# Kernel tuning notes

Measured on AMD Instinct MI355X. Metric: run time of the kernel, lower is better.

## Reference

```python
import jax, jax.numpy as jnp
import numpy as np

B, S, H, NH = 32, 577, 1024, 16
DH = H // NH


def setup_inputs() -> dict:
    key = jax.random.key(0)
    ks = jax.random.split(key, 10)
    s = 0.02
    return {
        "hidden_states": jax.random.normal(ks[0], (B, S, H), dtype=jnp.float32),
        "attention_mask": jnp.ones((B, S), dtype=jnp.float32),
        "Wq": jax.random.normal(ks[1], (H, H), dtype=jnp.float32) * s,
        "bq": jnp.zeros((H,), dtype=jnp.float32),
        "Wk": jax.random.normal(ks[2], (H, H), dtype=jnp.float32) * s,
        "bk": jnp.zeros((H,), dtype=jnp.float32),
        "Wv": jax.random.normal(ks[3], (H, H), dtype=jnp.float32) * s,
        "bv": jnp.zeros((H,), dtype=jnp.float32),
        "Wo": jax.random.normal(ks[4], (H, H), dtype=jnp.float32) * s,
        "bo": jnp.zeros((H,), dtype=jnp.float32),
    }


def reference(hidden_states, attention_mask, Wq, bq, Wk, bk, Wv, bv, Wo, bo):
    # torch nn.Linear: y = x @ W.T + b
    def heads(x):  # [B,S,H] -> [B,NH,S,DH]
        return x.reshape(B, S, NH, DH).transpose(0, 2, 1, 3)

    q = heads(hidden_states @ Wq.T + bq)
    k = heads(hidden_states @ Wk.T + bk)
    v = heads(hidden_states @ Wv.T + bv)

    scores = jnp.einsum("bhqd,bhkd->bhqk", q, k) / jnp.sqrt(jnp.float32(DH))
    # multiplicative mask, broadcast over heads and query positions
    scores = scores * attention_mask[:, None, None, :]
    probs = jax.nn.softmax(scores, axis=-1)
    ctx = jnp.einsum("bhqk,bhkd->bhqd", probs, v)
    ctx = ctx.transpose(0, 2, 1, 3).reshape(B, S, H)
    return ctx @ Wo.T + bo
```

## Files before the change

### kernel.cpp

```cpp
#include <hip/hip_runtime.h>
#include <hip/hip_bf16.h>


typedef __bf16 bf16_t;
typedef __bf16 bf16x8 __attribute__((ext_vector_type(8)));
typedef __bf16 bf16x4 __attribute__((ext_vector_type(4)));
typedef float f32x4 __attribute__((ext_vector_type(4)));

#define B_   32
#define S_   577
#define SP   608
#define H_   1024
#define NH_  16
#define DH_  64
#define M_   (B_ * S_)

typedef __attribute__((address_space(3))) unsigned int lds_u32;
typedef const __attribute__((address_space(1))) unsigned int glb_u32;
#define STAGE16(gp, lp) __builtin_amdgcn_global_load_lds((glb_u32*)(gp), (lds_u32*)(lp), 16, 0, 0)

__device__ __forceinline__ bf16x8 load8(const bf16_t* p) {
    return *reinterpret_cast<const bf16x8*>(p);
}
__device__ __forceinline__ bf16x8 load8f(const float* p) {
    f32x4 a = *reinterpret_cast<const f32x4*>(p);
    f32x4 b = *reinterpret_cast<const f32x4*>(p + 4);
    bf16x8 r;
    r[0] = (bf16_t)a[0]; r[1] = (bf16_t)a[1]; r[2] = (bf16_t)a[2]; r[3] = (bf16_t)a[3];
    r[4] = (bf16_t)b[0]; r[5] = (bf16_t)b[1]; r[6] = (bf16_t)b[2]; r[7] = (bf16_t)b[3];
    return r;
}

__global__ __launch_bounds__(256) void cvt_f32_bf16(const float* __restrict__ src,
                                                    bf16_t* __restrict__ dst, int n8)
{
    int i = blockIdx.x * blockDim.x + threadIdx.x;
    const int stride = gridDim.x * blockDim.x;
    for (; i < n8; i += stride)
        *reinterpret_cast<bf16x8*>(dst + (size_t)i * 8) = load8f(src + (size_t)i * 8);
}

__global__ __launch_bounds__(256) void cvt_w4(
    const float* __restrict__ s0, const float* __restrict__ s1,
    const float* __restrict__ s2, const float* __restrict__ s3,
    bf16_t* __restrict__ dst)
{
    const int i = blockIdx.x * blockDim.x + threadIdx.x;
    const int which = i >> 17;
    const int off = i & ((1 << 17) - 1);
    const float* s = (which == 0) ? s0 : (which == 1) ? s1 : (which == 2) ? s2 : s3;
    *reinterpret_cast<bf16x8*>(dst + (size_t)i * 8) = load8f(s + (size_t)off * 8);
}

#define GEMM_MAINLOOP(SWAP)                                                      \
    for (int k0 = 0; k0 < H_; k0 += 32) {                                        \
        STAGE16(pA0 + k0, lA0);                                                  \
        STAGE16(pA1 + k0, lA1);                                                  \
        STAGE16(pB0 + k0, lB0);                                                  \
        STAGE16(pB1 + k0, lB1);                                                  \
        __syncthreads();                                                         \
        bf16x8 af[4], bfv[4];                                                    \
        _Pragma("unroll")                                                        \
        for (int tt = 0; tt < 4; ++tt) {                                         \
            af[tt]  = load8(sA + (wm * 64 + tt * 16 + l16) * 32 + quad * 8);     \
            bfv[tt] = load8(sB + (wn * 64 + tt * 16 + l16) * 32 + quad * 8);     \
        }                                                                        \
        _Pragma("unroll")                                                        \
        for (int i = 0; i < 4; ++i)                                              \
            _Pragma("unroll")                                                    \
            for (int j = 0; j < 4; ++j)                                          \
                acc[i][j] = (SWAP)                                               \
                    ? __builtin_amdgcn_mfma_f32_16x16x32_bf16(bfv[j], af[i], acc[i][j], 0, 0, 0) \
                    : __builtin_amdgcn_mfma_f32_16x16x32_bf16(af[i], bfv[j], acc[i][j], 0, 0, 0); \
        __syncthreads();                                                         \
    }

__global__ __launch_bounds__(256) void qkv_gemm(
    const bf16_t* __restrict__ Xb,
    const bf16_t* __restrict__ Wqb, const bf16_t* __restrict__ Wkb, const bf16_t* __restrict__ Wvb,
    const float* __restrict__ bq, const float* __restrict__ bk, const float* __restrict__ bv,
    bf16_t* __restrict__ Qb, bf16_t* __restrict__ Kb, bf16_t* __restrict__ VTb)
{
    __shared__ bf16_t smem[8192];
    bf16_t* sA = smem;
    bf16_t* sB = smem + 4096;
    const int tid  = threadIdx.x;
    const int w    = tid >> 6, lane = tid & 63;
    const int quad = lane >> 4, l16 = lane & 15;
    const int wm = w & 1, wn = w >> 1;

    const int t    = (blockIdx.x & 7) * 435 + (blockIdx.x >> 3);
    const int slab = t / 192;
    const int rem  = t - slab * 192;
    int mt, nt;
    if (slab < 18) { nt = rem >> 3; mt = slab * 8 + (rem & 7); }
    else           { nt = rem;      mt = 144; }
    const int m0 = mt * 128, n0 = nt * 128;

    const int which = n0 >> 10;
    const int nrel0 = n0 & 1023;
    const bf16_t* Wb   = (which == 0) ? Wqb : (which == 1) ? Wkb : Wvb;
    const float*  bias = (which == 0) ? bq  : (which == 1) ? bk  : bv;
    const float   oscale = (which == 0) ? 0.125f : 1.0f;

    const int f0 = tid, f1 = 256 + tid;
    const int rA0 = f0 >> 2, cA0 = (f0 & 3) * 8;
    const int rA1 = f1 >> 2, cA1 = (f1 & 3) * 8;
    int ga0 = m0 + rA0; if (ga0 > M_ - 1) ga0 = M_ - 1;
    int ga1 = m0 + rA1; if (ga1 > M_ - 1) ga1 = M_ - 1;
    const bf16_t* pA0 = Xb + (size_t)ga0 * H_ + cA0;
    const bf16_t* pA1 = Xb + (size_t)ga1 * H_ + cA1;
    const bf16_t* pB0 = Wb + (size_t)(nrel0 + rA0) * H_ + cA0;
    const bf16_t* pB1 = Wb + (size_t)(nrel0 + rA1) * H_ + cA1;
    bf16_t* lA0 = sA + w * 512;
    bf16_t* lA1 = sA + 2048 + w * 512;
    bf16_t* lB0 = sB + w * 512;
    bf16_t* lB1 = sB + 2048 + w * 512;

    f32x4 acc[4][4] = {};
    if (which != 2) {
        GEMM_MAINLOOP(1)
        bf16_t* QKout = (which == 0) ? Qb : Kb;
#pragma unroll
        for (int j = 0; j < 4; ++j) {
            const int u  = wn * 4 + j;
            const int h  = (nrel0 >> 6) + (u >> 2);
            const int d0 = (u & 3) * 16 + quad * 4;
            const f32x4 b4 = *reinterpret_cast<const f32x4*>(&bias[nrel0 + u * 16 + quad * 4]);
#pragma unroll
            for (int i = 0; i < 4; ++i) {
                const int m = m0 + wm * 64 + i * 16 + l16;
                if (m >= M_) continue;
                const int b = m / S_, s = m - b * S_;
                const int bh = b * NH_ + h;
                bf16x4 pk;
#pragma unroll
                for (int r = 0; r < 4; ++r) pk[r] = (bf16_t)((acc[i][j][r] + b4[r]) * oscale);
                *reinterpret_cast<bf16x4*>(QKout + ((size_t)bh * S_ + s) * DH_ + d0) = pk;
            }
        }
    } else {
        GEMM_MAINLOOP(0)
#pragma unroll
        for (int j = 0; j < 4; ++j) {
            const int nrel = nrel0 + wn * 64 + j * 16 + l16;
            const float bv_ = bias[nrel];
            const int h = nrel >> 6, d = nrel & 63;
#pragma unroll
            for (int i = 0; i < 4; ++i) {
                const int m = m0 + wm * 64 + i * 16 + quad * 4;
                const int b = m / S_, s = m - b * S_;
                if (m + 3 < M_ && s <= S_ - 4) {
                    bf16x4 pk;
#pragma unroll
                    for (int r = 0; r < 4; ++r) pk[r] = (bf16_t)(acc[i][j][r] + bv_);
                    *reinterpret_cast<bf16x4*>(VTb + ((size_t)(b * NH_ + h) * DH_ + d) * SP + s) = pk;
                } else {
#pragma unroll
                    for (int r = 0; r < 4; ++r) {
                        const int mm = m + r;
                        if (mm >= M_) continue;
                        const int bb = mm / S_, ss = mm - bb * S_;
                        VTb[((size_t)(bb * NH_ + h) * DH_ + d) * SP + ss] = (bf16_t)(acc[i][j][r] + bv_);
                    }
                }
            }
        }
    }
}

__global__ __launch_bounds__(256, 3) void flash_attn(
    const bf16_t* __restrict__ Qb, const bf16_t* __restrict__ Kb,
    const bf16_t* __restrict__ VTb, const float* __restrict__ maskp,
    bf16_t* __restrict__ Ctx)
{
    __shared__ __align__(16) float smask[SP];
    const int tid  = threadIdx.x;
    const int w    = tid >> 6, lane = tid & 63;
    const int quad = lane >> 4, l16 = lane & 15;

    const int bid  = blockIdx.x;
    const int work = (bid & 7) * 320 + (bid >> 3);
    const int bh   = work / 5;
    const int qx   = work - bh * 5;
    const int b    = bh >> 4, h = bh & 15;

    for (int i = tid; i < SP; i += 256)
        smask[i] = (i < S_) ? maskp[b * S_ + i] : 0.f;
    __syncthreads();

    int idx = qx * 4 + w; if (idx > 18) idx = 18;
    const int q0 = idx * 32;

    const bf16_t* Qh = Qb  + (size_t)bh * S_ * DH_;
    const bf16_t* Kh = Kb  + (size_t)bh * S_ * DH_;
    const bf16_t* Vh = VTb + (size_t)bh * DH_ * SP;

    int rqA = q0 + l16;      if (rqA > S_ - 1) rqA = S_ - 1;
    int rqB = q0 + 16 + l16; if (rqB > S_ - 1) rqB = S_ - 1;
    const bf16x8 aqA0 = load8(Qh + rqA * DH_ + quad * 8);
    const bf16x8 aqA1 = load8(Qh + rqA * DH_ + 32 + quad * 8);
    const bf16x8 aqB0 = load8(Qh + rqB * DH_ + quad * 8);
    const bf16x8 aqB1 = load8(Qh + rqB * DH_ + 32 + quad * 8);

    const int g0 = ((l16 >> 2) << 3) + (l16 & 3);
    const int g1 = g0 + 4;

    f32x4 oA[4] = {}, oB[4] = {};
    float lpA = 0.f, lpB = 0.f;

    bf16x8 ka[4], kb_[4];
    {
        int r0 = g0; if (r0 > S_ - 1) r0 = S_ - 1;
        int r1 = g1; if (r1 > S_ - 1) r1 = S_ - 1;
        ka[0] = load8(Kh + r0 * DH_ + quad * 8);
        ka[1] = load8(Kh + r0 * DH_ + 32 + quad * 8);
        ka[2] = load8(Kh + r1 * DH_ + quad * 8);
        ka[3] = load8(Kh + r1 * DH_ + 32 + quad * 8);
    }

    auto body = [&](bf16x8 (&KC)[4], bf16x8 (&KN)[4], const int j0, const bool pf) {
        bf16x8 v0 = load8(Vh + (l16)      * SP + j0 + quad * 8);
        bf16x8 v1 = load8(Vh + (16 + l16) * SP + j0 + quad * 8);
        bf16x8 v2 = load8(Vh + (32 + l16) * SP + j0 + quad * 8);
        bf16x8 v3 = load8(Vh + (48 + l16) * SP + j0 + quad * 8);
        if (pf) {
            int r0 = j0 + 32 + g0; if (r0 > S_ - 1) r0 = S_ - 1;
            int r1 = j0 + 32 + g1; if (r1 > S_ - 1) r1 = S_ - 1;
            KN[0] = load8(Kh + r0 * DH_ + quad * 8);
            KN[1] = load8(Kh + r0 * DH_ + 32 + quad * 8);
            KN[2] = load8(Kh + r1 * DH_ + quad * 8);
            KN[3] = load8(Kh + r1 * DH_ + 32 + quad * 8);
        }
        f32x4 sA0 = {}, sA1 = {}, sB0 = {}, sB1 = {};
        sA0 = __builtin_amdgcn_mfma_f32_16x16x32_bf16(KC[0], aqA0, sA0, 0, 0, 0);
        sA0 = __builtin_amdgcn_mfma_f32_16x16x32_bf16(KC[1], aqA1, sA0, 0, 0, 0);
        sA1 = __builtin_amdgcn_mfma_f32_16x16x32_bf16(KC[2], aqA0, sA1, 0, 0, 0);
        sA1 = __builtin_amdgcn_mfma_f32_16x16x32_bf16(KC[3], aqA1, sA1, 0, 0, 0);
        sB0 = __builtin_amdgcn_mfma_f32_16x16x32_bf16(KC[0], aqB0, sB0, 0, 0, 0);
        sB0 = __builtin_amdgcn_mfma_f32_16x16x32_bf16(KC[1], aqB1, sB0, 0, 0, 0);
        sB1 = __builtin_amdgcn_mfma_f32_16x16x32_bf16(KC[2], aqB0, sB1, 0, 0, 0);
        sB1 = __builtin_amdgcn_mfma_f32_16x16x32_bf16(KC[3], aqB1, sB1, 0, 0, 0);

        const f32x4 mk0 = *reinterpret_cast<const f32x4*>(&smask[j0 + quad * 8]);
        const f32x4 mk1 = *reinterpret_cast<const f32x4*>(&smask[j0 + quad * 8 + 4]);
        bf16x8 apA, apB;
#pragma unroll
        for (int r = 0; r < 4; ++r) {
            const int c0 = j0 + quad * 8 + r;
            const int c1 = c0 + 4;
            const float eA0 = (c0 < S_) ? __expf(sA0[r] * mk0[r]) : 0.f;
            const float eA1 = (c1 < S_) ? __expf(sA1[r] * mk1[r]) : 0.f;
            const float eB0 = (c0 < S_) ? __expf(sB0[r] * mk0[r]) : 0.f;
            const float eB1 = (c1 < S_) ? __expf(sB1[r] * mk1[r]) : 0.f;
            lpA += eA0 + eA1;
            lpB += eB0 + eB1;
            apA[r] = (bf16_t)eA0; apA[r + 4] = (bf16_t)eA1;
            apB[r] = (bf16_t)eB0; apB[r + 4] = (bf16_t)eB1;
        }
        oA[0] = __builtin_amdgcn_mfma_f32_16x16x32_bf16(apA, v0, oA[0], 0, 0, 0);
        oB[0] = __builtin_amdgcn_mfma_f32_16x16x32_bf16(apB, v0, oB[0], 0, 0, 0);
        oA[1] = __builtin_amdgcn_mfma_f32_16x16x32_bf16(apA, v1, oA[1], 0, 0, 0);
        oB[1] = __builtin_amdgcn_mfma_f32_16x16x32_bf16(apB, v1, oB[1], 0, 0, 0);
        oA[2] = __builtin_amdgcn_mfma_f32_16x16x32_bf16(apA, v2, oA[2], 0, 0, 0);
        oB[2] = __builtin_amdgcn_mfma_f32_16x16x32_bf16(apB, v2, oB[2], 0, 0, 0);
        oA[3] = __builtin_amdgcn_mfma_f32_16x16x32_bf16(apA, v3, oA[3], 0, 0, 0);
        oB[3] = __builtin_amdgcn_mfma_f32_16x16x32_bf16(apB, v3, oB[3], 0, 0, 0);
    };

    for (int j0 = 0; j0 < S_; j0 += 64) {
        body(ka, kb_, j0, j0 + 32 < S_);
        if (j0 + 32 < S_) body(kb_, ka, j0 + 32, j0 + 64 < S_);
    }

    float lsA = lpA, lsB = lpB;
    lsA += __shfl_xor(lsA, 16); lsA += __shfl_xor(lsA, 32);
    lsB += __shfl_xor(lsB, 16); lsB += __shfl_xor(lsB, 32);
    float livA[4], livB[4];
#pragma unroll
    for (int r = 0; r < 4; ++r) {
        livA[r] = 1.0f / __shfl(lsA, quad * 4 + r);
        livB[r] = 1.0f / __shfl(lsB, quad * 4 + r);
    }

#pragma unroll
    for (int t = 0; t < 4; ++t) {
#pragma unroll
        for (int r = 0; r < 4; ++r) {
            const int sA = q0 + quad * 4 + r;
            const int sB = sA + 16;
            if (sA < S_)
                Ctx[((size_t)(b * S_ + sA) * NH_ + h) * DH_ + t * 16 + l16] =
                    (bf16_t)(oA[t][r] * livA[r]);
            if (sB < S_)
                Ctx[((size_t)(b * S_ + sB) * NH_ + h) * DH_ + t * 16 + l16] =
                    (bf16_t)(oB[t][r] * livB[r]);
        }
    }
}

__global__ __launch_bounds__(256) void out_gemm(
    const bf16_t* __restrict__ Ctx, const bf16_t* __restrict__ Wob,
    const float* __restrict__ bo, float* __restrict__ Out)
{
    __shared__ bf16_t smem[8192];
    bf16_t* sA = smem;
    bf16_t* sB = smem + 4096;
    const int tid  = threadIdx.x;
    const int w    = tid >> 6, lane = tid & 63;
    const int quad = lane >> 4, l16 = lane & 15;
    const int wm = w & 1, wn = w >> 1;

    const int t    = (blockIdx.x & 7) * 145 + (blockIdx.x >> 3);
    const int slab = t / 64;
    const int rem  = t - slab * 64;
    int mt, nt;
    if (slab < 18) { nt = rem >> 3; mt = slab * 8 + (rem & 7); }
    else           { nt = rem;      mt = 144; }
    const int m0 = mt * 128, n0 = nt * 128;

    const int f0 = tid, f1 = 256 + tid;
    const int rA0 = f0 >> 2, cA0 = (f0 & 3) * 8;
    const int rA1 = f1 >> 2, cA1 = (f1 & 3) * 8;
    int ga0 = m0 + rA0; if (ga0 > M_ - 1) ga0 = M_ - 1;
    int ga1 = m0 + rA1; if (ga1 > M_ - 1) ga1 = M_ - 1;
    const bf16_t* pA0 = Ctx + (size_t)ga0 * H_ + cA0;
    const bf16_t* pA1 = Ctx + (size_t)ga1 * H_ + cA1;
    const bf16_t* pB0 = Wob + (size_t)(n0 + rA0) * H_ + cA0;
    const bf16_t* pB1 = Wob + (size_t)(n0 + rA1) * H_ + cA1;
    bf16_t* lA0 = sA + w * 512;
    bf16_t* lA1 = sA + 2048 + w * 512;
    bf16_t* lB0 = sB + w * 512;
    bf16_t* lB1 = sB + 2048 + w * 512;

    f32x4 acc[4][4] = {};
    GEMM_MAINLOOP(1)

#pragma unroll
    for (int j = 0; j < 4; ++j) {
        const int nb = n0 + wn * 64 + j * 16 + quad * 4;
        const f32x4 b4 = *reinterpret_cast<const f32x4*>(&bo[nb]);
#pragma unroll
        for (int i = 0; i < 4; ++i) {
            const int m = m0 + wm * 64 + i * 16 + l16;
            if (m >= M_) continue;
            f32x4 v = acc[i][j] + b4;
            *reinterpret_cast<f32x4*>(Out + (size_t)m * H_ + nb) = v;
        }
    }
}

extern "C" void kernel_launch(void* const* d_in, const int* in_sizes, int n_in,
                              void* d_out, int out_size, void* d_ws, size_t ws_size,
                              hipStream_t stream) {
    const float* hidden = (const float*)d_in[0];
    const float* mask   = (const float*)d_in[1];
    const float* Wq = (const float*)d_in[2];
    const float* bq = (const float*)d_in[3];
    const float* Wk = (const float*)d_in[4];
    const float* bk = (const float*)d_in[5];
    const float* Wv = (const float*)d_in[6];
    const float* bv = (const float*)d_in[7];
    const float* Wo = (const float*)d_in[8];
    const float* bo = (const float*)d_in[9];
    float* out = (float*)d_out;

    const size_t QK_EL = (size_t)B_ * NH_ * S_ * DH_;
    const size_t VT_EL = (size_t)B_ * NH_ * SP * DH_;
    const size_t X_EL  = (size_t)M_ * H_;
    const size_t W_EL  = (size_t)H_ * H_;
    const size_t NEED  = (2 * QK_EL + VT_EL + X_EL + 4 * W_EL) * sizeof(bf16_t);
    if (ws_size < NEED) {
        hipMemsetAsync(d_out, 0, (size_t)out_size * sizeof(float), stream);
        return;
    }

    bf16_t* ws    = (bf16_t*)d_ws;
    bf16_t* Qb    = ws;
    bf16_t* Kb    = Qb + QK_EL;
    bf16_t* VTb   = Kb + QK_EL;
    bf16_t* XbCtx = VTb + VT_EL;
    bf16_t* Wqb   = XbCtx + X_EL;
    bf16_t* Wkb   = Wqb + W_EL;
    bf16_t* Wvb   = Wkb + W_EL;
    bf16_t* Wob   = Wvb + W_EL;

    cvt_f32_bf16<<<2048, 256, 0, stream>>>(hidden, XbCtx, (int)(X_EL / 8));
    cvt_w4<<<2048, 256, 0, stream>>>(Wq, Wk, Wv, Wo, Wqb);

    qkv_gemm<<<dim3(3480), dim3(256), 0, stream>>>(XbCtx, Wqb, Wkb, Wvb, bq, bk, bv, Qb, Kb, VTb);

    flash_attn<<<dim3(2560), dim3(256), 0, stream>>>(Qb, Kb, VTb, mask, XbCtx);

    out_gemm<<<dim3(1160), dim3(256), 0, stream>>>(XbCtx, Wob, bo, out);
}
```

Before: 504.9 us.

## Double-buffer LDS staging in GEMMs and raise wave priority around attention MFMAs

The GEMM main loop now uses two LDS buffers, so the global-to-LDS load for the next K-slice is issued before the MFMAs on the current slice run, and one of the two barriers per step is removed. Shared memory per block doubles to 32 KB, which may lower occupancy. The attention kernel also wraps its MFMA groups in s_setprio(1)/s_setprio(0) so waves issuing matrix work are favoured by the scheduler over waves doing softmax and loads.

```diff
diff --git a/kernel.cpp b/kernel.cpp
--- a/kernel.cpp
+++ b/kernel.cpp
@@ -52,18 +52,21 @@
     *reinterpret_cast<bf16x8*>(dst + (size_t)i * 8) = load8f(s + (size_t)off * 8);
 }
 
-#define GEMM_MAINLOOP(SWAP)                                                      \
-    for (int k0 = 0; k0 < H_; k0 += 32) {                                        \
-        STAGE16(pA0 + k0, lA0);                                                  \
-        STAGE16(pA1 + k0, lA1);                                                  \
-        STAGE16(pB0 + k0, lB0);                                                  \
-        STAGE16(pB1 + k0, lB1);                                                  \
-        __syncthreads();                                                         \
+#define GEMM_STAGE(base, kofs)                                                   \
+    do {                                                                         \
+        STAGE16(pA0 + (kofs), (base) + w * 512);                                 \
+        STAGE16(pA1 + (kofs), (base) + 2048 + w * 512);                          \
+        STAGE16(pB0 + (kofs), (base) + 4096 + w * 512);                          \
+        STAGE16(pB1 + (kofs), (base) + 6144 + w * 512);                          \
+    } while (0)
+
+#define GEMM_COMPUTE(base, SWAP)                                                 \
+    do {                                                                         \
         bf16x8 af[4], bfv[4];                                                    \
         _Pragma("unroll")                                                        \
         for (int tt = 0; tt < 4; ++tt) {                                         \
-            af[tt]  = load8(sA + (wm * 64 + tt * 16 + l16) * 32 + quad * 8);     \
-            bfv[tt] = load8(sB + (wn * 64 + tt * 16 + l16) * 32 + quad * 8);     \
+            af[tt]  = load8((base) + (wm * 64 + tt * 16 + l16) * 32 + quad * 8); \
+            bfv[tt] = load8((base) + 4096 + (wn * 64 + tt * 16 + l16) * 32 + quad * 8); \
         }                                                                        \
         _Pragma("unroll")                                                        \
         for (int i = 0; i < 4; ++i)                                              \
@@ -72,6 +75,17 @@
                 acc[i][j] = (SWAP)                                               \
                     ? __builtin_amdgcn_mfma_f32_16x16x32_bf16(bfv[j], af[i], acc[i][j], 0, 0, 0) \
                     : __builtin_amdgcn_mfma_f32_16x16x32_bf16(af[i], bfv[j], acc[i][j], 0, 0, 0); \
+    } while (0)
+
+#define GEMM_MAINLOOP(SWAP)                                                      \
+    GEMM_STAGE(smem, 0);                                                         \
+    __syncthreads();                                                             \
+    for (int kk = 0; kk < H_; kk += 64) {                                        \
+        GEMM_STAGE(smem + 8192, kk + 32);                                        \
+        GEMM_COMPUTE(smem, SWAP);                                                \
+        __syncthreads();                                                         \
+        if (kk + 64 < H_) GEMM_STAGE(smem, kk + 64);                             \
+        GEMM_COMPUTE(smem + 8192, SWAP);                                         \
         __syncthreads();                                                         \
     }
 
@@ -81,9 +95,7 @@
     const float* __restrict__ bq, const float* __restrict__ bk, const float* __restrict__ bv,
     bf16_t* __restrict__ Qb, bf16_t* __restrict__ Kb, bf16_t* __restrict__ VTb)
 {
-    __shared__ bf16_t smem[8192];
-    bf16_t* sA = smem;
-    bf16_t* sB = smem + 4096;
+    __shared__ bf16_t smem[16384];
     const int tid  = threadIdx.x;
     const int w    = tid >> 6, lane = tid & 63;
     const int quad = lane >> 4, l16 = lane & 15;
@@ -112,10 +124,6 @@
     const bf16_t* pA1 = Xb + (size_t)ga1 * H_ + cA1;
     const bf16_t* pB0 = Wb + (size_t)(nrel0 + rA0) * H_ + cA0;
     const bf16_t* pB1 = Wb + (size_t)(nrel0 + rA1) * H_ + cA1;
-    bf16_t* lA0 = sA + w * 512;
-    bf16_t* lA1 = sA + 2048 + w * 512;
-    bf16_t* lB0 = sB + w * 512;
-    bf16_t* lB1 = sB + 2048 + w * 512;
 
     f32x4 acc[4][4] = {};
     if (which != 2) {
@@ -233,6 +241,7 @@
             KN[3] = load8(Kh + r1 * DH_ + 32 + quad * 8);
         }
         f32x4 sA0 = {}, sA1 = {}, sB0 = {}, sB1 = {};
+        __builtin_amdgcn_s_setprio(1);
         sA0 = __builtin_amdgcn_mfma_f32_16x16x32_bf16(KC[0], aqA0, sA0, 0, 0, 0);
         sA0 = __builtin_amdgcn_mfma_f32_16x16x32_bf16(KC[1], aqA1, sA0, 0, 0, 0);
         sA1 = __builtin_amdgcn_mfma_f32_16x16x32_bf16(KC[2], aqA0, sA1, 0, 0, 0);
@@ -241,6 +250,7 @@
         sB0 = __builtin_amdgcn_mfma_f32_16x16x32_bf16(KC[1], aqB1, sB0, 0, 0, 0);
         sB1 = __builtin_amdgcn_mfma_f32_16x16x32_bf16(KC[2], aqB0, sB1, 0, 0, 0);
         sB1 = __builtin_amdgcn_mfma_f32_16x16x32_bf16(KC[3], aqB1, sB1, 0, 0, 0);
+        __builtin_amdgcn_s_setprio(0);
 
         const f32x4 mk0 = *reinterpret_cast<const f32x4*>(&smask[j0 + quad * 8]);
         const f32x4 mk1 = *reinterpret_cast<const f32x4*>(&smask[j0 + quad * 8 + 4]);
@@ -258,6 +268,7 @@
             apA[r] = (bf16_t)eA0; apA[r + 4] = (bf16_t)eA1;
             apB[r] = (bf16_t)eB0; apB[r + 4] = (bf16_t)eB1;
         }
+        __builtin_amdgcn_s_setprio(1);
         oA[0] = __builtin_amdgcn_mfma_f32_16x16x32_bf16(apA, v0, oA[0], 0, 0, 0);
         oB[0] = __builtin_amdgcn_mfma_f32_16x16x32_bf16(apB, v0, oB[0], 0, 0, 0);
         oA[1] = __builtin_amdgcn_mfma_f32_16x16x32_bf16(apA, v1, oA[1], 0, 0, 0);
@@ -266,6 +277,7 @@
         oB[2] = __builtin_amdgcn_mfma_f32_16x16x32_bf16(apB, v2, oB[2], 0, 0, 0);
         oA[3] = __builtin_amdgcn_mfma_f32_16x16x32_bf16(apA, v3, oA[3], 0, 0, 0);
         oB[3] = __builtin_amdgcn_mfma_f32_16x16x32_bf16(apB, v3, oB[3], 0, 0, 0);
+        __builtin_amdgcn_s_setprio(0);
     };
 
     for (int j0 = 0; j0 < S_; j0 += 64) {
@@ -303,9 +315,7 @@
     const bf16_t* __restrict__ Ctx, const bf16_t* __restrict__ Wob,
     const float* __restrict__ bo, float* __restrict__ Out)
 {
-    __shared__ bf16_t smem[8192];
-    bf16_t* sA = smem;
-    bf16_t* sB = smem + 4096;
+    __shared__ bf16_t smem[16384];
     const int tid  = threadIdx.x;
     const int w    = tid >> 6, lane = tid & 63;
     const int quad = lane >> 4, l16 = lane & 15;
@@ -328,10 +338,6 @@
     const bf16_t* pA1 = Ctx + (size_t)ga1 * H_ + cA1;
     const bf16_t* pB0 = Wob + (size_t)(n0 + rA0) * H_ + cA0;
     const bf16_t* pB1 = Wob + (size_t)(n0 + rA1) * H_ + cA1;
-    bf16_t* lA0 = sA + w * 512;
-    bf16_t* lA1 = sA + 2048 + w * 512;
-    bf16_t* lB0 = sB + w * 512;
-    bf16_t* lB1 = sB + 2048 + w * 512;
 
     f32x4 acc[4][4] = {};
     GEMM_MAINLOOP(1)
```

New measurement: 507.7 us. Within noise of the previous version (+0.6%).

## Rewrite QKV GEMM with 256x256 tiles and multi-stage async LDS pipeline

Applied to the files above, without the earlier changes.

Replaces the QKV projection GEMM's 128x128 single-buffered main loop with a 256x256 tile using 512 threads and a four-slot LDS ring (two K-halves by two parities). Global-to-LDS loads for future steps are issued while MFMAs run, and waits use explicit vmcnt counts instead of full syncthreads. The grid is remapped across XCDs to match the new tile count. s_setprio is also raised around the MFMA bursts in the GEMM and the flash attention kernel. The larger tile cuts load traffic per FLOP and hides load latency, at the cost of 128KB of LDS and higher register pressure, which may lower occupancy.

```diff
diff --git a/kernel.cpp b/kernel.cpp
--- a/kernel.cpp
+++ b/kernel.cpp
@@ -18,6 +18,7 @@
 typedef __attribute__((address_space(3))) unsigned int lds_u32;
 typedef const __attribute__((address_space(1))) unsigned int glb_u32;
 #define STAGE16(gp, lp) __builtin_amdgcn_global_load_lds((glb_u32*)(gp), (lds_u32*)(lp), 16, 0, 0)
+#define MFMA_BF16 __builtin_amdgcn_mfma_f32_16x16x32_bf16
 
 __device__ __forceinline__ bf16x8 load8(const bf16_t* p) {
     return *reinterpret_cast<const bf16x8*>(p);
@@ -52,50 +53,91 @@
     *reinterpret_cast<bf16x8*>(dst + (size_t)i * 8) = load8f(s + (size_t)off * 8);
 }
 
-#define GEMM_MAINLOOP(SWAP)                                                      \
-    for (int k0 = 0; k0 < H_; k0 += 32) {                                        \
-        STAGE16(pA0 + k0, lA0);                                                  \
-        STAGE16(pA1 + k0, lA1);                                                  \
-        STAGE16(pB0 + k0, lB0);                                                  \
-        STAGE16(pB1 + k0, lB1);                                                  \
-        __syncthreads();                                                         \
-        bf16x8 af[4], bfv[4];                                                    \
+#define AR(par, kk) (((par) * 2 + (kk)) * 8192)
+#define BR(par, kk) (32768 + ((par) * 2 + (kk)) * 8192)
+
+#define STG_A(par, kk, T)                                                        \
+    do {                                                                         \
+        STAGE16(pA0 + (T) * 64 + (kk) * 32, smem + AR(par, kk) + w * 512);       \
+        STAGE16(pA1 + (T) * 64 + (kk) * 32, smem + AR(par, kk) + 4096 + w * 512);\
+    } while (0)
+#define STG_B(par, kk, T)                                                        \
+    do {                                                                         \
+        STAGE16(pB0 + (T) * 64 + (kk) * 32, smem + BR(par, kk) + w * 512);       \
+        STAGE16(pB1 + (T) * 64 + (kk) * 32, smem + BR(par, kk) + 4096 + w * 512);\
+    } while (0)
+
+#define PHASE_A(par, kk, STG, SWAP)                                              \
+    do {                                                                         \
+        asm volatile("s_waitcnt vmcnt(8)" ::: "memory");                         \
+        __builtin_amdgcn_s_barrier();                                            \
+        STG;                                                                     \
         _Pragma("unroll")                                                        \
-        for (int tt = 0; tt < 4; ++tt) {                                         \
-            af[tt]  = load8(sA + (wm * 64 + tt * 16 + l16) * 32 + quad * 8);     \
-            bfv[tt] = load8(sB + (wn * 64 + tt * 16 + l16) * 32 + quad * 8);     \
+        for (int i = 0; i < 8; ++i)                                              \
+            af[i] = load8(smem + AR(par, kk) + (wr * 128 + i * 16 + l16) * 32 + quad * 8); \
+        bfv[0] = load8(smem + BR(par, kk) + (wc * 64 + l16) * 32 + quad * 8);    \
+        bfv[1] = load8(smem + BR(par, kk) + (wc * 64 + 16 + l16) * 32 + quad * 8); \
+        __builtin_amdgcn_s_setprio(1);                                           \
+        _Pragma("unroll")                                                        \
+        for (int i = 0; i < 8; ++i) {                                            \
+            acc[i][0] = (SWAP) ? MFMA_BF16(bfv[0], af[i], acc[i][0], 0, 0, 0)    \
+                               : MFMA_BF16(af[i], bfv[0], acc[i][0], 0, 0, 0);   \
+            acc[i][1] = (SWAP) ? MFMA_BF16(bfv[1], af[i], acc[i][1], 0, 0, 0)    \
+                               : MFMA_BF16(af[i], bfv[1], acc[i][1], 0, 0, 0);   \
         }                                                                        \
+        __builtin_amdgcn_s_setprio(0);                                           \
+    } while (0)
+
+#define PHASE_B(par, kk, STG, SWAP)                                              \
+    do {                                                                         \
+        STG;                                                                     \
+        bfv[2] = load8(smem + BR(par, kk) + (wc * 64 + 32 + l16) * 32 + quad * 8); \
+        bfv[3] = load8(smem + BR(par, kk) + (wc * 64 + 48 + l16) * 32 + quad * 8); \
+        __builtin_amdgcn_s_setprio(1);                                           \
         _Pragma("unroll")                                                        \
-        for (int i = 0; i < 4; ++i)                                              \
-            _Pragma("unroll")                                                    \
-            for (int j = 0; j < 4; ++j)                                          \
-                acc[i][j] = (SWAP)                                               \
-                    ? __builtin_amdgcn_mfma_f32_16x16x32_bf16(bfv[j], af[i], acc[i][j], 0, 0, 0) \
-                    : __builtin_amdgcn_mfma_f32_16x16x32_bf16(af[i], bfv[j], acc[i][j], 0, 0, 0); \
-        __syncthreads();                                                         \
-    }
-
-__global__ __launch_bounds__(256) void qkv_gemm(
+        for (int i = 0; i < 8; ++i) {                                            \
+            acc[i][2] = (SWAP) ? MFMA_BF16(bfv[2], af[i], acc[i][2], 0, 0, 0)    \
+                               : MFMA_BF16(af[i], bfv[2], acc[i][2], 0, 0, 0);   \
+            acc[i][3] = (SWAP) ? MFMA_BF16(bfv[3], af[i], acc[i][3], 0, 0, 0)    \
+                               : MFMA_BF16(af[i], bfv[3], acc[i][3], 0, 0, 0);   \
+        }                                                                        \
+        __builtin_amdgcn_s_setprio(0);                                           \
+    } while (0)
+
+#define QKV_MAIN(SWAP)                                                           \
+    STG_A(0, 0, 0); STG_B(0, 0, 0); STG_A(0, 1, 0); STG_B(0, 1, 0);              \
+    STG_A(1, 0, 1); STG_B(1, 0, 1);                                              \
+    for (int it = 0; it < 8; ++it) {                                             \
+        const int t1 = 2 * it + 1;                                               \
+        const int t2 = (2 * it + 2 < 16) ? 2 * it + 2 : 15;                      \
+        const int t3 = (2 * it + 3 < 16) ? 2 * it + 3 : 15;                      \
+        PHASE_A(0, 0, STG_A(1, 1, t1), SWAP); PHASE_B(0, 0, STG_B(1, 1, t1), SWAP); \
+        PHASE_A(0, 1, STG_A(0, 0, t2), SWAP); PHASE_B(0, 1, STG_B(0, 0, t2), SWAP); \
+        PHASE_A(1, 0, STG_A(0, 1, t2), SWAP); PHASE_B(1, 0, STG_B(0, 1, t2), SWAP); \
+        PHASE_A(1, 1, STG_A(1, 0, t3), SWAP); PHASE_B(1, 1, STG_B(1, 0, t3), SWAP); \
+    }                                                                            \
+    asm volatile("s_waitcnt vmcnt(0)" ::: "memory");
+
+__global__ __launch_bounds__(512, 2) void qkv_gemm(
     const bf16_t* __restrict__ Xb,
     const bf16_t* __restrict__ Wqb, const bf16_t* __restrict__ Wkb, const bf16_t* __restrict__ Wvb,
     const float* __restrict__ bq, const float* __restrict__ bk, const float* __restrict__ bv,
     bf16_t* __restrict__ Qb, bf16_t* __restrict__ Kb, bf16_t* __restrict__ VTb)
 {
-    __shared__ bf16_t smem[8192];
-    bf16_t* sA = smem;
-    bf16_t* sB = smem + 4096;
+    __shared__ bf16_t smem[65536];
     const int tid  = threadIdx.x;
     const int w    = tid >> 6, lane = tid & 63;
     const int quad = lane >> 4, l16 = lane & 15;
-    const int wm = w & 1, wn = w >> 1;
-
-    const int t    = (blockIdx.x & 7) * 435 + (blockIdx.x >> 3);
-    const int slab = t / 192;
-    const int rem  = t - slab * 192;
+    const int wr = w >> 2, wc = w & 3;
+
+    const int orig = blockIdx.x;
+    const int xcd = orig & 7, lin = orig >> 3;
+    const int work = (xcd < 4 ? xcd * 110 : 440 + (xcd - 4) * 109) + lin;
     int mt, nt;
-    if (slab < 18) { nt = rem >> 3; mt = slab * 8 + (rem & 7); }
-    else           { nt = rem;      mt = 144; }
-    const int m0 = mt * 128, n0 = nt * 128;
+    if (work < 864) { const int slab = work / 48, rem = work - slab * 48;
+                      nt = rem >> 2; mt = slab * 4 + (rem & 3); }
+    else            { nt = work - 864; mt = 72; }
+    const int m0 = mt * 256, n0 = nt * 256;
 
     const int which = n0 >> 10;
     const int nrel0 = n0 & 1023;
@@ -103,33 +145,28 @@
     const float*  bias = (which == 0) ? bq  : (which == 1) ? bk  : bv;
     const float   oscale = (which == 0) ? 0.125f : 1.0f;
 
-    const int f0 = tid, f1 = 256 + tid;
-    const int rA0 = f0 >> 2, cA0 = (f0 & 3) * 8;
-    const int rA1 = f1 >> 2, cA1 = (f1 & 3) * 8;
-    int ga0 = m0 + rA0; if (ga0 > M_ - 1) ga0 = M_ - 1;
-    int ga1 = m0 + rA1; if (ga1 > M_ - 1) ga1 = M_ - 1;
-    const bf16_t* pA0 = Xb + (size_t)ga0 * H_ + cA0;
-    const bf16_t* pA1 = Xb + (size_t)ga1 * H_ + cA1;
-    const bf16_t* pB0 = Wb + (size_t)(nrel0 + rA0) * H_ + cA0;
-    const bf16_t* pB1 = Wb + (size_t)(nrel0 + rA1) * H_ + cA1;
-    bf16_t* lA0 = sA + w * 512;
-    bf16_t* lA1 = sA + 2048 + w * 512;
-    bf16_t* lB0 = sB + w * 512;
-    bf16_t* lB1 = sB + 2048 + w * 512;
-
-    f32x4 acc[4][4] = {};
+    const int srow = tid >> 2, scol = (tid & 3) * 8;
+    int ga0 = m0 + srow;       if (ga0 > M_ - 1) ga0 = M_ - 1;
+    int ga1 = m0 + 128 + srow; if (ga1 > M_ - 1) ga1 = M_ - 1;
+    const bf16_t* pA0 = Xb + (size_t)ga0 * H_ + scol;
+    const bf16_t* pA1 = Xb + (size_t)ga1 * H_ + scol;
+    const bf16_t* pB0 = Wb + (size_t)(nrel0 + srow) * H_ + scol;
+    const bf16_t* pB1 = Wb + (size_t)(nrel0 + 128 + srow) * H_ + scol;
+
+    bf16x8 af[8], bfv[4];
+    f32x4 acc[8][4] = {};
+
     if (which != 2) {
-        GEMM_MAINLOOP(1)
+        QKV_MAIN(1)
         bf16_t* QKout = (which == 0) ? Qb : Kb;
 #pragma unroll
         for (int j = 0; j < 4; ++j) {
-            const int u  = wn * 4 + j;
-            const int h  = (nrel0 >> 6) + (u >> 2);
-            const int d0 = (u & 3) * 16 + quad * 4;
-            const f32x4 b4 = *reinterpret_cast<const f32x4*>(&bias[nrel0 + u * 16 + quad * 4]);
-#pragma unroll
-            for (int i = 0; i < 4; ++i) {
-                const int m = m0 + wm * 64 + i * 16 + l16;
+            const int nrelj = nrel0 + wc * 64 + j * 16 + quad * 4;
+            const int h = nrelj >> 6, d0 = nrelj & 63;
+            const f32x4 b4 = *reinterpret_cast<const f32x4*>(&bias[nrelj]);
+#pragma unroll
+            for (int i = 0; i < 8; ++i) {
+                const int m = m0 + wr * 128 + i * 16 + l16;
                 if (m >= M_) continue;
                 const int b = m / S_, s = m - b * S_;
                 const int bh = b * NH_ + h;
@@ -140,15 +177,15 @@
             }
         }
     } else {
-        GEMM_MAINLOOP(0)
+        QKV_MAIN(0)
 #pragma unroll
         for (int j = 0; j < 4; ++j) {
-            const int nrel = nrel0 + wn * 64 + j * 16 + l16;
-            const float bv_ = bias[nrel];
-            const int h = nrel >> 6, d = nrel & 63;
-#pragma unroll
-            for (int i = 0; i < 4; ++i) {
-                const int m = m0 + wm * 64 + i * 16 + quad * 4;
+            const int nrelj = nrel0 + wc * 64 + j * 16 + l16;
+            const int h = nrelj >> 6, d = nrelj & 63;
+            const float bv_ = bias[nrelj];
+#pragma unroll
+            for (int i = 0; i < 8; ++i) {
+                const int m = m0 + wr * 128 + i * 16 + quad * 4;
                 const int b = m / S_, s = m - b * S_;
                 if (m + 3 < M_ && s <= S_ - 4) {
                     bf16x4 pk;
@@ -233,14 +270,16 @@
             KN[3] = load8(Kh + r1 * DH_ + 32 + quad * 8);
         }
         f32x4 sA0 = {}, sA1 = {}, sB0 = {}, sB1 = {};
-        sA0 = __builtin_amdgcn_mfma_f32_16x16x32_bf16(KC[0], aqA0, sA0, 0, 0, 0);
-        sA0 = __builtin_amdgcn_mfma_f32_16x16x32_bf16(KC[1], aqA1, sA0, 0, 0, 0);
-        sA1 = __builtin_amdgcn_mfma_f32_16x16x32_bf16(KC[2], aqA0, sA1, 0, 0, 0);
-        sA1 = __builtin_amdgcn_mfma_f32_16x16x32_bf16(KC[3], aqA1, sA1, 0, 0, 0);
-        sB0 = __builtin_amdgcn_mfma_f32_16x16x32_bf16(KC[0], aqB0, sB0, 0, 0, 0);
-        sB0 = __builtin_amdgcn_mfma_f32_16x16x32_bf16(KC[1], aqB1, sB0, 0, 0, 0);
-        sB1 = __builtin_amdgcn_mfma_f32_16x16x32_bf16(KC[2], aqB0, sB1, 0, 0, 0);
-        sB1 = __builtin_amdgcn_mfma_f32_16x16x32_bf16(KC[3], aqB1, sB1, 0, 0, 0);
+        __builtin_amdgcn_s_setprio(1);
+        sA0 = MFMA_BF16(KC[0], aqA0, sA0, 0, 0, 0);
+        sA0 = MFMA_BF16(KC[1], aqA1, sA0, 0, 0, 0);
+        sA1 = MFMA_BF16(KC[2], aqA0, sA1, 0, 0, 0);
+        sA1 = MFMA_BF16(KC[3], aqA1, sA1, 0, 0, 0);
+        sB0 = MFMA_BF16(KC[0], aqB0, sB0, 0, 0, 0);
+        sB0 = MFMA_BF16(KC[1], aqB1, sB0, 0, 0, 0);
+        sB1 = MFMA_BF16(KC[2], aqB0, sB1, 0, 0, 0);
+        sB1 = MFMA_BF16(KC[3], aqB1, sB1, 0, 0, 0);
+        __builtin_amdgcn_s_setprio(0);
 
         const f32x4 mk0 = *reinterpret_cast<const f32x4*>(&smask[j0 + quad * 8]);
         const f32x4 mk1 = *reinterpret_cast<const f32x4*>(&smask[j0 + quad * 8 + 4]);
@@ -258,14 +297,16 @@
             apA[r] = (bf16_t)eA0; apA[r + 4] = (bf16_t)eA1;
             apB[r] = (bf16_t)eB0; apB[r + 4] = (bf16_t)eB1;
         }
-        oA[0] = __builtin_amdgcn_mfma_f32_16x16x32_bf16(apA, v0, oA[0], 0, 0, 0);
-        oB[0] = __builtin_amdgcn_mfma_f32_16x16x32_bf16(apB, v0, oB[0], 0, 0, 0);
-        oA[1] = __builtin_amdgcn_mfma_f32_16x16x32_bf16(apA, v1, oA[1], 0, 0, 0);
-        oB[1] = __builtin_amdgcn_mfma_f32_16x16x32_bf16(apB, v1, oB[1], 0, 0, 0);
-        oA[2] = __builtin_amdgcn_mfma_f32_16x16x32_bf16(apA, v2, oA[2], 0, 0, 0);
-        oB[2] = __builtin_amdgcn_mfma_f32_16x16x32_bf16(apB, v2, oB[2], 0, 0, 0);
-        oA[3] = __builtin_amdgcn_mfma_f32_16x16x32_bf16(apA, v3, oA[3], 0, 0, 0);
-        oB[3] = __builtin_amdgcn_mfma_f32_16x16x32_bf16(apB, v3, oB[3], 0, 0, 0);
+        __builtin_amdgcn_s_setprio(1);
+        oA[0] = MFMA_BF16(apA, v0, oA[0], 0, 0, 0);
+        oB[0] = MFMA_BF16(apB, v0, oB[0], 0, 0, 0);
+        oA[1] = MFMA_BF16(apA, v1, oA[1], 0, 0, 0);
+        oB[1] = MFMA_BF16(apB, v1, oB[1], 0, 0, 0);
+        oA[2] = MFMA_BF16(apA, v2, oA[2], 0, 0, 0);
+        oB[2] = MFMA_BF16(apB, v2, oB[2], 0, 0, 0);
+        oA[3] = MFMA_BF16(apA, v3, oA[3], 0, 0, 0);
+        oB[3] = MFMA_BF16(apB, v3, oB[3], 0, 0, 0);
+        __builtin_amdgcn_s_setprio(0);
     };
 
     for (int j0 = 0; j0 < S_; j0 += 64) {
@@ -334,7 +375,25 @@
     bf16_t* lB1 = sB + 2048 + w * 512;
 
     f32x4 acc[4][4] = {};
-    GEMM_MAINLOOP(1)
+    for (int k0 = 0; k0 < H_; k0 += 32) {
+        STAGE16(pA0 + k0, lA0);
+        STAGE16(pA1 + k0, lA1);
+        STAGE16(pB0 + k0, lB0);
+        STAGE16(pB1 + k0, lB1);
+        __syncthreads();
+        bf16x8 af[4], bfv[4];
+#pragma unroll
+        for (int tt = 0; tt < 4; ++tt) {
+            af[tt]  = load8(sA + (wm * 64 + tt * 16 + l16) * 32 + quad * 8);
+            bfv[tt] = load8(sB + (wn * 64 + tt * 16 + l16) * 32 + quad * 8);
+        }
+#pragma unroll
+        for (int i = 0; i < 4; ++i)
+#pragma unroll
+            for (int j = 0; j < 4; ++j)
+                acc[i][j] = MFMA_BF16(bfv[j], af[i], acc[i][j], 0, 0, 0);
+        __syncthreads();
+    }
 
 #pragma unroll
     for (int j = 0; j < 4; ++j) {
@@ -388,7 +447,7 @@
     cvt_f32_bf16<<<2048, 256, 0, stream>>>(hidden, XbCtx, (int)(X_EL / 8));
     cvt_w4<<<2048, 256, 0, stream>>>(Wq, Wk, Wv, Wo, Wqb);
 
-    qkv_gemm<<<dim3(3480), dim3(256), 0, stream>>>(XbCtx, Wqb, Wkb, Wvb, bq, bk, bv, Qb, Kb, VTb);
+    qkv_gemm<<<dim3(876), dim3(512), 0, stream>>>(XbCtx, Wqb, Wkb, Wvb, bq, bk, bv, Qb, Kb, VTb);
 
     flash_attn<<<dim3(2560), dim3(256), 0, stream>>>(Qb, Kb, VTb, mask, XbCtx);
 
```

Result: no change. 511.5 us (+1.3%).

## Widen attention wave tile to 64 queries and merge conversion kernels

Applied to the files above, without the earlier changes.

Each flash-attention wave now handles 64 query rows (four 16-row tiles) instead of 32. Every K and V fragment loaded from global memory is reused across twice as many MFMAs, which halves K/V traffic per query. The grid shrinks to 1536 blocks with occupancy lowered to 2 per SIMD, and s_setprio is wrapped around the MFMA bursts. The two fp32-to-bf16 conversion kernels are merged into one launch to save launch overhead. In exchange, the larger tile raises register pressure and lowers occupancy, and the last query chunk does more clamped redundant work.

```diff
diff --git a/kernel.cpp b/kernel.cpp
--- a/kernel.cpp
+++ b/kernel.cpp
@@ -18,6 +18,7 @@
 typedef __attribute__((address_space(3))) unsigned int lds_u32;
 typedef const __attribute__((address_space(1))) unsigned int glb_u32;
 #define STAGE16(gp, lp) __builtin_amdgcn_global_load_lds((glb_u32*)(gp), (lds_u32*)(lp), 16, 0, 0)
+#define MFMA_BF16 __builtin_amdgcn_mfma_f32_16x16x32_bf16
 
 __device__ __forceinline__ bf16x8 load8(const bf16_t* p) {
     return *reinterpret_cast<const bf16x8*>(p);
@@ -31,25 +32,25 @@
     return r;
 }
 
-__global__ __launch_bounds__(256) void cvt_f32_bf16(const float* __restrict__ src,
-                                                    bf16_t* __restrict__ dst, int n8)
+__global__ __launch_bounds__(256) void cvt_all(
+    const float* __restrict__ x,
+    const float* __restrict__ w0, const float* __restrict__ w1,
+    const float* __restrict__ w2, const float* __restrict__ w3,
+    bf16_t* __restrict__ xdst, bf16_t* __restrict__ wdst, int xn8)
 {
     int i = blockIdx.x * blockDim.x + threadIdx.x;
     const int stride = gridDim.x * blockDim.x;
-    for (; i < n8; i += stride)
-        *reinterpret_cast<bf16x8*>(dst + (size_t)i * 8) = load8f(src + (size_t)i * 8);
-}
-
-__global__ __launch_bounds__(256) void cvt_w4(
-    const float* __restrict__ s0, const float* __restrict__ s1,
-    const float* __restrict__ s2, const float* __restrict__ s3,
-    bf16_t* __restrict__ dst)
-{
-    const int i = blockIdx.x * blockDim.x + threadIdx.x;
-    const int which = i >> 17;
-    const int off = i & ((1 << 17) - 1);
-    const float* s = (which == 0) ? s0 : (which == 1) ? s1 : (which == 2) ? s2 : s3;
-    *reinterpret_cast<bf16x8*>(dst + (size_t)i * 8) = load8f(s + (size_t)off * 8);
+    const int total = xn8 + 4 * (1 << 17);
+    for (; i < total; i += stride) {
+        if (i < xn8) {
+            *reinterpret_cast<bf16x8*>(xdst + (size_t)i * 8) = load8f(x + (size_t)i * 8);
+        } else {
+            const int j = i - xn8;
+            const int which = j >> 17, off = j & ((1 << 17) - 1);
+            const float* s = (which == 0) ? w0 : (which == 1) ? w1 : (which == 2) ? w2 : w3;
+            *reinterpret_cast<bf16x8*>(wdst + (size_t)j * 8) = load8f(s + (size_t)off * 8);
+        }
+    }
 }
 
 #define GEMM_MAINLOOP(SWAP)                                                      \
@@ -70,8 +71,8 @@
             _Pragma("unroll")                                                    \
             for (int j = 0; j < 4; ++j)                                          \
                 acc[i][j] = (SWAP)                                               \
-                    ? __builtin_amdgcn_mfma_f32_16x16x32_bf16(bfv[j], af[i], acc[i][j], 0, 0, 0) \
-                    : __builtin_amdgcn_mfma_f32_16x16x32_bf16(af[i], bfv[j], acc[i][j], 0, 0, 0); \
+                    ? MFMA_BF16(bfv[j], af[i], acc[i][j], 0, 0, 0)               \
+                    : MFMA_BF16(af[i], bfv[j], acc[i][j], 0, 0, 0);              \
         __syncthreads();                                                         \
     }
 
@@ -169,7 +170,7 @@
     }
 }
 
-__global__ __launch_bounds__(256, 3) void flash_attn(
+__global__ __launch_bounds__(256, 2) void flash_attn(
     const bf16_t* __restrict__ Qb, const bf16_t* __restrict__ Kb,
     const bf16_t* __restrict__ VTb, const float* __restrict__ maskp,
     bf16_t* __restrict__ Ctx)
@@ -180,34 +181,35 @@
     const int quad = lane >> 4, l16 = lane & 15;
 
     const int bid  = blockIdx.x;
-    const int work = (bid & 7) * 320 + (bid >> 3);
-    const int bh   = work / 5;
-    const int qx   = work - bh * 5;
+    const int work = (bid & 7) * 192 + (bid >> 3);
+    const int bh   = work / 3;
+    const int qx   = work - bh * 3;
     const int b    = bh >> 4, h = bh & 15;
 
     for (int i = tid; i < SP; i += 256)
         smask[i] = (i < S_) ? maskp[b * S_ + i] : 0.f;
     __syncthreads();
 
-    int idx = qx * 4 + w; if (idx > 18) idx = 18;
-    const int q0 = idx * 32;
+    int idx = qx * 4 + w; if (idx > 9) idx = 9;
+    const int q0 = idx * 64;
 
     const bf16_t* Qh = Qb  + (size_t)bh * S_ * DH_;
     const bf16_t* Kh = Kb  + (size_t)bh * S_ * DH_;
     const bf16_t* Vh = VTb + (size_t)bh * DH_ * SP;
 
-    int rqA = q0 + l16;      if (rqA > S_ - 1) rqA = S_ - 1;
-    int rqB = q0 + 16 + l16; if (rqB > S_ - 1) rqB = S_ - 1;
-    const bf16x8 aqA0 = load8(Qh + rqA * DH_ + quad * 8);
-    const bf16x8 aqA1 = load8(Qh + rqA * DH_ + 32 + quad * 8);
-    const bf16x8 aqB0 = load8(Qh + rqB * DH_ + quad * 8);
-    const bf16x8 aqB1 = load8(Qh + rqB * DH_ + 32 + quad * 8);
+    bf16x8 aq[4][2];
+#pragma unroll
+    for (int t = 0; t < 4; ++t) {
+        int rq = q0 + t * 16 + l16; if (rq > S_ - 1) rq = S_ - 1;
+        aq[t][0] = load8(Qh + rq * DH_ + quad * 8);
+        aq[t][1] = load8(Qh + rq * DH_ + 32 + quad * 8);
+    }
 
     const int g0 = ((l16 >> 2) << 3) + (l16 & 3);
     const int g1 = g0 + 4;
 
-    f32x4 oA[4] = {}, oB[4] = {};
-    float lpA = 0.f, lpB = 0.f;
+    f32x4 o[4][4] = {};
+    float lp[4] = {0.f, 0.f, 0.f, 0.f};
 
     bf16x8 ka[4], kb_[4];
     {
@@ -232,40 +234,43 @@
             KN[2] = load8(Kh + r1 * DH_ + quad * 8);
             KN[3] = load8(Kh + r1 * DH_ + 32 + quad * 8);
         }
-        f32x4 sA0 = {}, sA1 = {}, sB0 = {}, sB1 = {};
-        sA0 = __builtin_amdgcn_mfma_f32_16x16x32_bf16(KC[0], aqA0, sA0, 0, 0, 0);
-        sA0 = __builtin_amdgcn_mfma_f32_16x16x32_bf16(KC[1], aqA1, sA0, 0, 0, 0);
-        sA1 = __builtin_amdgcn_mfma_f32_16x16x32_bf16(KC[2], aqA0, sA1, 0, 0, 0);
-        sA1 = __builtin_amdgcn_mfma_f32_16x16x32_bf16(KC[3], aqA1, sA1, 0, 0, 0);
-        sB0 = __builtin_amdgcn_mfma_f32_16x16x32_bf16(KC[0], aqB0, sB0, 0, 0, 0);
-        sB0 = __builtin_amdgcn_mfma_f32_16x16x32_bf16(KC[1], aqB1, sB0, 0, 0, 0);
-        sB1 = __builtin_amdgcn_mfma_f32_16x16x32_bf16(KC[2], aqB0, sB1, 0, 0, 0);
-        sB1 = __builtin_amdgcn_mfma_f32_16x16x32_bf16(KC[3], aqB1, sB1, 0, 0, 0);
+        f32x4 s0[4], s1[4];
+        __builtin_amdgcn_s_setprio(1);
+#pragma unroll
+        for (int t = 0; t < 4; ++t) {
+            f32x4 z0 = {}, z1 = {};
+            z0 = MFMA_BF16(KC[0], aq[t][0], z0, 0, 0, 0);
+            z0 = MFMA_BF16(KC[1], aq[t][1], z0, 0, 0, 0);
+            z1 = MFMA_BF16(KC[2], aq[t][0], z1, 0, 0, 0);
+            z1 = MFMA_BF16(KC[3], aq[t][1], z1, 0, 0, 0);
+            s0[t] = z0; s1[t] = z1;
+        }
+        __builtin_amdgcn_s_setprio(0);
 
         const f32x4 mk0 = *reinterpret_cast<const f32x4*>(&smask[j0 + quad * 8]);
         const f32x4 mk1 = *reinterpret_cast<const f32x4*>(&smask[j0 + quad * 8 + 4]);
-        bf16x8 apA, apB;
-#pragma unroll
-        for (int r = 0; r < 4; ++r) {
-            const int c0 = j0 + quad * 8 + r;
-            const int c1 = c0 + 4;
-            const float eA0 = (c0 < S_) ? __expf(sA0[r] * mk0[r]) : 0.f;
-            const float eA1 = (c1 < S_) ? __expf(sA1[r] * mk1[r]) : 0.f;
-            const float eB0 = (c0 < S_) ? __expf(sB0[r] * mk0[r]) : 0.f;
-            const float eB1 = (c1 < S_) ? __expf(sB1[r] * mk1[r]) : 0.f;
-            lpA += eA0 + eA1;
-            lpB += eB0 + eB1;
-            apA[r] = (bf16_t)eA0; apA[r + 4] = (bf16_t)eA1;
-            apB[r] = (bf16_t)eB0; apB[r + 4] = (bf16_t)eB1;
-        }
-        oA[0] = __builtin_amdgcn_mfma_f32_16x16x32_bf16(apA, v0, oA[0], 0, 0, 0);
-        oB[0] = __builtin_amdgcn_mfma_f32_16x16x32_bf16(apB, v0, oB[0], 0, 0, 0);
-        oA[1] = __builtin_amdgcn_mfma_f32_16x16x32_bf16(apA, v1, oA[1], 0, 0, 0);
-        oB[1] = __builtin_amdgcn_mfma_f32_16x16x32_bf16(apB, v1, oB[1], 0, 0, 0);
-        oA[2] = __builtin_amdgcn_mfma_f32_16x16x32_bf16(apA, v2, oA[2], 0, 0, 0);
-        oB[2] = __builtin_amdgcn_mfma_f32_16x16x32_bf16(apB, v2, oB[2], 0, 0, 0);
-        oA[3] = __builtin_amdgcn_mfma_f32_16x16x32_bf16(apA, v3, oA[3], 0, 0, 0);
-        oB[3] = __builtin_amdgcn_mfma_f32_16x16x32_bf16(apB, v3, oB[3], 0, 0, 0);
+        bf16x8 ap[4];
+#pragma unroll
+        for (int t = 0; t < 4; ++t) {
+#pragma unroll
+            for (int r = 0; r < 4; ++r) {
+                const int c0 = j0 + quad * 8 + r;
+                const int c1 = c0 + 4;
+                const float e0 = (c0 < S_) ? __expf(s0[t][r] * mk0[r]) : 0.f;
+                const float e1 = (c1 < S_) ? __expf(s1[t][r] * mk1[r]) : 0.f;
+                lp[t] += e0 + e1;
+                ap[t][r] = (bf16_t)e0; ap[t][r + 4] = (bf16_t)e1;
+            }
+        }
+        __builtin_amdgcn_s_setprio(1);
+#pragma unroll
+        for (int t = 0; t < 4; ++t) {
+            o[t][0] = MFMA_BF16(ap[t], v0, o[t][0], 0, 0, 0);
+            o[t][1] = MFMA_BF16(ap[t], v1, o[t][1], 0, 0, 0);
+            o[t][2] = MFMA_BF16(ap[t], v2, o[t][2], 0, 0, 0);
+            o[t][3] = MFMA_BF16(ap[t], v3, o[t][3], 0, 0, 0);
+        }
+        __builtin_amdgcn_s_setprio(0);
     };
 
     for (int j0 = 0; j0 < S_; j0 += 64) {
@@ -273,28 +278,27 @@
         if (j0 + 32 < S_) body(kb_, ka, j0 + 32, j0 + 64 < S_);
     }
 
-    float lsA = lpA, lsB = lpB;
-    lsA += __shfl_xor(lsA, 16); lsA += __shfl_xor(lsA, 32);
-    lsB += __shfl_xor(lsB, 16); lsB += __shfl_xor(lsB, 32);
-    float livA[4], livB[4];
-#pragma unroll
-    for (int r = 0; r < 4; ++r) {
-        livA[r] = 1.0f / __shfl(lsA, quad * 4 + r);
-        livB[r] = 1.0f / __shfl(lsB, quad * 4 + r);
-    }
-
+    float liv[4][4];
 #pragma unroll
     for (int t = 0; t < 4; ++t) {
-#pragma unroll
-        for (int r = 0; r < 4; ++r) {
-            const int sA = q0 + quad * 4 + r;
-            const int sB = sA + 16;
-            if (sA < S_)
-                Ctx[((size_t)(b * S_ + sA) * NH_ + h) * DH_ + t * 16 + l16] =
-                    (bf16_t)(oA[t][r] * livA[r]);
-            if (sB < S_)
-                Ctx[((size_t)(b * S_ + sB) * NH_ + h) * DH_ + t * 16 + l16] =
-                    (bf16_t)(oB[t][r] * livB[r]);
+        float ls = lp[t];
+        ls += __shfl_xor(ls, 16); ls += __shfl_xor(ls, 32);
+#pragma unroll
+        for (int r = 0; r < 4; ++r)
+            liv[t][r] = 1.0f / __shfl(ls, quad * 4 + r);
+    }
+
+#pragma unroll
+    for (int t = 0; t < 4; ++t) {
+#pragma unroll
+        for (int dt = 0; dt < 4; ++dt) {
+#pragma unroll
+            for (int r = 0; r < 4; ++r) {
+                const int s = q0 + t * 16 + quad * 4 + r;
+                if (s < S_)
+                    Ctx[((size_t)(b * S_ + s) * NH_ + h) * DH_ + dt * 16 + l16] =
+                        (bf16_t)(o[t][dt][r] * liv[t][r]);
+            }
         }
     }
 }
@@ -385,12 +389,11 @@
     bf16_t* Wvb   = Wkb + W_EL;
     bf16_t* Wob   = Wvb + W_EL;
 
-    cvt_f32_bf16<<<2048, 256, 0, stream>>>(hidden, XbCtx, (int)(X_EL / 8));
-    cvt_w4<<<2048, 256, 0, stream>>>(Wq, Wk, Wv, Wo, Wqb);
+    cvt_all<<<2048, 256, 0, stream>>>(hidden, Wq, Wk, Wv, Wo, XbCtx, Wqb, (int)(X_EL / 8));
 
     qkv_gemm<<<dim3(3480), dim3(256), 0, stream>>>(XbCtx, Wqb, Wkb, Wvb, bq, bk, bv, Qb, Kb, VTb);
 
-    flash_attn<<<dim3(2560), dim3(256), 0, stream>>>(Qb, Kb, VTb, mask, XbCtx);
+    flash_attn<<<dim3(1536), dim3(256), 0, stream>>>(Qb, Kb, VTb, mask, XbCtx);
 
     out_gemm<<<dim3(1160), dim3(256), 0, stream>>>(XbCtx, Wob, bo, out);
 }
```

Result: faster. 470.1 us (-6.9%).
